# Kernel tuning notes

Hardware: AMD Instinct MI355X
Metric: run time of the kernel (lower is better)

## Reference

```python
import jax, jax.numpy as jnp
import numpy as np

OUT_GRID = (256, 256)  # output_grid_shape


def setup_inputs() -> dict:
    key = jax.random.key(0)
    k1, k2 = jax.random.split(key)
    N, H, W, C = 16, 256, 256, 32
    x = jax.random.normal(k1, (N, H, W, C), dtype=jnp.float32)
    # loc network: global mean pool -> dense(6); small weights + identity-affine bias
    W_loc = jax.random.normal(k2, (C, 6), dtype=jnp.float32) * 0.01
    b_loc = jnp.array([1.0, 0.0, 0.0, 0.0, 1.0, 0.0], dtype=jnp.float32)
    return {"x": x, "W_loc": W_loc, "b_loc": b_loc}


def _spatial_transform(x, W_loc, b_loc):
    N, H, W, C = x.shape
    Ho, Wo = OUT_GRID
    # loc_network: params (N, 6) -> theta (N, 2, 3)
    params = jnp.mean(x, axis=(1, 2)) @ W_loc + b_loc
    theta = params.reshape(N, 2, 3)
    # grid_transform_fn: affine on [-1,1]-normalized output index grid
    gy = jnp.linspace(-1.0, 1.0, Ho, dtype=jnp.float32)
    gx = jnp.linspace(-1.0, 1.0, Wo, dtype=jnp.float32)
    Gy, Gx = jnp.meshgrid(gy, gx, indexing="ij")
    grid = jnp.stack([Gy.ravel(), Gx.ravel(), jnp.ones(Ho * Wo, jnp.float32)], axis=0)  # (3, Ho*Wo)
    coords = jnp.einsum("npq,qm->npm", theta, grid).reshape(N, 2, Ho, Wo)  # in ~[-1,1]
    # interpolate_bilinear with clip (wrap=False)
    maxes = jnp.array([H - 1, W - 1], dtype=jnp.float32)
    up = (coords + 1.0) * maxes[None, :, None, None] * 0.5  # upscale to pixel coords
    f = jnp.floor(up)
    frac = up - f  # (N, 2, Ho, Wo)
    fi = f.astype(jnp.int32)
    batch = jnp.arange(N)[:, None, None]
    out = jnp.zeros((N, Ho, Wo, C), dtype=x.dtype)
    for by in (0, 1):  # 2^dim corner offsets (bitfield)
        for bx in (0, 1):
            cy = jnp.clip(fi[:, 0] + by, 0, H - 1)
            cx = jnp.clip(fi[:, 1] + bx, 0, W - 1)
            wy = frac[:, 0] if by else 1.0 - frac[:, 0]
            wx = frac[:, 1] if bx else 1.0 - frac[:, 1]
            out = out + x[batch, cy, cx] * (wy * wx)[..., None]
    return out


def reference(x, W_loc, b_loc):
    return _spatial_transform(x, W_loc, b_loc)
```

## Files before the change

kernel.cpp:

```cpp
#include <hip/hip_runtime.h>


#define NIMG 16
#define HDIM 256
#define WDIM 256
#define CH   32
#define HW   (HDIM * WDIM)
#define BPI  128

typedef float f32x4 __attribute__((ext_vector_type(4)));

__global__ __launch_bounds__(256) void st_sum_kernel(
    const float* __restrict__ x, float* __restrict__ partials) {
    const int n   = blockIdx.x >> 7;
    const int blk = blockIdx.x & (BPI - 1);
    const int tid = threadIdx.x;
    const int cg  = tid & 7;
    const int sp  = tid >> 3;

    const float4* xp = (const float4*)(x + (size_t)n * HW * CH);
    float4 a0 = make_float4(0.f, 0.f, 0.f, 0.f);
    float4 a1 = make_float4(0.f, 0.f, 0.f, 0.f);
    int s = blk * 32 + sp;
    #pragma unroll
    for (int it = 0; it < 8; ++it) {
        float4 v0 = xp[(size_t)s * 8 + cg];
        float4 v1 = xp[(size_t)(s + BPI * 32) * 8 + cg];
        a0.x += v0.x; a0.y += v0.y; a0.z += v0.z; a0.w += v0.w;
        a1.x += v1.x; a1.y += v1.y; a1.z += v1.z; a1.w += v1.w;
        s += BPI * 64;
    }
    a0.x += a1.x; a0.y += a1.y; a0.z += a1.z; a0.w += a1.w;

    __shared__ float4 red[256];
    red[tid] = a0;
    __syncthreads();
    for (int stride = 16; stride >= 1; stride >>= 1) {
        if (sp < stride) {
            float4 o = red[(sp + stride) * 8 + cg];
            a0.x += o.x; a0.y += o.y; a0.z += o.z; a0.w += o.w;
            red[tid] = a0;
        }
        __syncthreads();
    }
    if (sp == 0) {
        ((float4*)(partials + ((size_t)blk * NIMG + n) * CH))[cg] = a0;
    }
}

__global__ __launch_bounds__(512) void st_theta_kernel(
    const float* __restrict__ partials, const float* __restrict__ W_loc,
    const float* __restrict__ b_loc, float* __restrict__ theta) {
    __shared__ float mean[NIMG * CH];
    const int t = threadIdx.x;
    float s = 0.f;
    for (int b = 0; b < BPI; ++b) s += partials[b * NIMG * CH + t];
    mean[t] = s * (1.0f / (float)HW);
    __syncthreads();
    if (t < NIMG * 6) {
        const int n = t / 6, k = t % 6;
        float acc = b_loc[k];
        for (int c = 0; c < CH; ++c)
            acc = fmaf(mean[n * CH + c], W_loc[c * 6 + k], acc);
        theta[t] = acc;
    }
}

__global__ __launch_bounds__(256) void st_interp_kernel(
    const float* __restrict__ x, const float* __restrict__ theta,
    float* __restrict__ out) {
    const int bid = (int)blockIdx.x;
    const int swz = (bid & 7) * 2048 + (bid >> 3);
    const int n   = swz >> 10;
    const int r   = swz & 1023;
    const int ty  = r >> 4;
    const int tx  = r & 15;
    const int tid = threadIdx.x;
    const int p   = tid >> 3;
    const int cg  = tid & 7;

    const int ho  = ty * 4 + (p >> 3);
    const int wo0 = tx * 16 + (p & 7);
    const int wo1 = wo0 + 8;

    const float* th = theta + n * 6;
    const float t00 = th[0], t01 = th[1], t02 = th[2];
    const float t10 = th[3], t11 = th[4], t12 = th[5];

    const float gy = fmaf((float)ho, 2.0f / 255.0f, -1.0f);
    const float gx0 = fmaf((float)wo0, 2.0f / 255.0f, -1.0f);
    const float gx1 = fmaf((float)wo1, 2.0f / 255.0f, -1.0f);

    const float uyA = (fmaf(t00, gy, fmaf(t01, gx0, t02)) + 1.0f) * 127.5f;
    const float uxA = (fmaf(t10, gy, fmaf(t11, gx0, t12)) + 1.0f) * 127.5f;
    const float uyB = (fmaf(t00, gy, fmaf(t01, gx1, t02)) + 1.0f) * 127.5f;
    const float uxB = (fmaf(t10, gy, fmaf(t11, gx1, t12)) + 1.0f) * 127.5f;

    const float fyA = floorf(uyA), fxA = floorf(uxA);
    const float fyB = floorf(uyB), fxB = floorf(uxB);
    const float ryA = uyA - fyA, rxA = uxA - fxA;
    const float ryB = uyB - fyB, rxB = uxB - fxB;

    const int iyA0 = min(max((int)fyA,     0), HDIM - 1);
    const int iyA1 = min(max((int)fyA + 1, 0), HDIM - 1);
    const int ixA0 = min(max((int)fxA,     0), WDIM - 1);
    const int ixA1 = min(max((int)fxA + 1, 0), WDIM - 1);
    const int iyB0 = min(max((int)fyB,     0), HDIM - 1);
    const int iyB1 = min(max((int)fyB + 1, 0), HDIM - 1);
    const int ixB0 = min(max((int)fxB,     0), WDIM - 1);
    const int ixB1 = min(max((int)fxB + 1, 0), WDIM - 1);

    const float4* xp = (const float4*)(x + (size_t)n * HW * CH);
    float4 a00 = xp[(size_t)(iyA0 * WDIM + ixA0) * 8 + cg];
    float4 a01 = xp[(size_t)(iyA0 * WDIM + ixA1) * 8 + cg];
    float4 a10 = xp[(size_t)(iyA1 * WDIM + ixA0) * 8 + cg];
    float4 a11 = xp[(size_t)(iyA1 * WDIM + ixA1) * 8 + cg];
    float4 b00 = xp[(size_t)(iyB0 * WDIM + ixB0) * 8 + cg];
    float4 b01 = xp[(size_t)(iyB0 * WDIM + ixB1) * 8 + cg];
    float4 b10 = xp[(size_t)(iyB1 * WDIM + ixB0) * 8 + cg];
    float4 b11 = xp[(size_t)(iyB1 * WDIM + ixB1) * 8 + cg];

    const float wA00 = (1.0f - ryA) * (1.0f - rxA);
    const float wA01 = (1.0f - ryA) * rxA;
    const float wA10 = ryA * (1.0f - rxA);
    const float wA11 = ryA * rxA;
    const float wB00 = (1.0f - ryB) * (1.0f - rxB);
    const float wB01 = (1.0f - ryB) * rxB;
    const float wB10 = ryB * (1.0f - rxB);
    const float wB11 = ryB * rxB;

    f32x4 oA, oB;
    oA.x = a00.x * wA00 + a01.x * wA01 + a10.x * wA10 + a11.x * wA11;
    oA.y = a00.y * wA00 + a01.y * wA01 + a10.y * wA10 + a11.y * wA11;
    oA.z = a00.z * wA00 + a01.z * wA01 + a10.z * wA10 + a11.z * wA11;
    oA.w = a00.w * wA00 + a01.w * wA01 + a10.w * wA10 + a11.w * wA11;
    oB.x = b00.x * wB00 + b01.x * wB01 + b10.x * wB10 + b11.x * wB11;
    oB.y = b00.y * wB00 + b01.y * wB01 + b10.y * wB10 + b11.y * wB11;
    oB.z = b00.z * wB00 + b01.z * wB01 + b10.z * wB10 + b11.z * wB11;
    oB.w = b00.w * wB00 + b01.w * wB01 + b10.w * wB10 + b11.w * wB11;

    f32x4* op = (f32x4*)(out + (size_t)n * HW * CH);
    __builtin_nontemporal_store(oA, &op[(size_t)(ho * WDIM + wo0) * 8 + cg]);
    __builtin_nontemporal_store(oB, &op[(size_t)(ho * WDIM + wo1) * 8 + cg]);
}

extern "C" void kernel_launch(void* const* d_in, const int* in_sizes, int n_in,
                              void* d_out, int out_size, void* d_ws, size_t ws_size,
                              hipStream_t stream) {
    const float* x     = (const float*)d_in[0];
    const float* W_loc = (const float*)d_in[1];
    const float* b_loc = (const float*)d_in[2];
    float* out = (float*)d_out;

    float* partials = (float*)d_ws;
    float* theta    = partials + BPI * NIMG * CH;

    st_sum_kernel<<<NIMG * BPI, 256, 0, stream>>>(x, partials);
    st_theta_kernel<<<1, 512, 0, stream>>>(partials, W_loc, b_loc, theta);
    st_interp_kernel<<<NIMG * (HW / 64), 256, 0, stream>>>(x, theta, out);
}
```

Baseline: 68.66 us.

## Fuse theta computation into interpolation kernel and halve sum-kernel block count

Removes the single-block theta kernel launch. Each interpolation block now reduces the per-image partial sums itself and computes its own 6 affine parameters in shared memory. The sum kernel uses 64 blocks per image, each with four independent accumulators, so half as many partials are written. This saves a launch and the serial tail of a one-block kernel, at the cost of redundant partial reads and extra syncs in all 16384 interpolation blocks.

```diff
diff --git a/kernel.cpp b/kernel.cpp
--- a/kernel.cpp
+++ b/kernel.cpp
@@ -6,13 +6,13 @@
 #define WDIM 256
 #define CH   32
 #define HW   (HDIM * WDIM)
-#define BPI  128
+#define BPI  64
 
 typedef float f32x4 __attribute__((ext_vector_type(4)));
 
 __global__ __launch_bounds__(256) void st_sum_kernel(
     const float* __restrict__ x, float* __restrict__ partials) {
-    const int n   = blockIdx.x >> 7;
+    const int n   = blockIdx.x >> 6;
     const int blk = blockIdx.x & (BPI - 1);
     const int tid = threadIdx.x;
     const int cg  = tid & 7;
@@ -21,16 +21,24 @@
     const float4* xp = (const float4*)(x + (size_t)n * HW * CH);
     float4 a0 = make_float4(0.f, 0.f, 0.f, 0.f);
     float4 a1 = make_float4(0.f, 0.f, 0.f, 0.f);
+    float4 a2 = make_float4(0.f, 0.f, 0.f, 0.f);
+    float4 a3 = make_float4(0.f, 0.f, 0.f, 0.f);
     int s = blk * 32 + sp;
     #pragma unroll
     for (int it = 0; it < 8; ++it) {
-        float4 v0 = xp[(size_t)s * 8 + cg];
-        float4 v1 = xp[(size_t)(s + BPI * 32) * 8 + cg];
+        float4 v0 = xp[(size_t)(s       ) * 8 + cg];
+        float4 v1 = xp[(size_t)(s + 2048) * 8 + cg];
+        float4 v2 = xp[(size_t)(s + 4096) * 8 + cg];
+        float4 v3 = xp[(size_t)(s + 6144) * 8 + cg];
         a0.x += v0.x; a0.y += v0.y; a0.z += v0.z; a0.w += v0.w;
         a1.x += v1.x; a1.y += v1.y; a1.z += v1.z; a1.w += v1.w;
-        s += BPI * 64;
+        a2.x += v2.x; a2.y += v2.y; a2.z += v2.z; a2.w += v2.w;
+        a3.x += v3.x; a3.y += v3.y; a3.z += v3.z; a3.w += v3.w;
+        s += 8192;
     }
     a0.x += a1.x; a0.y += a1.y; a0.z += a1.z; a0.w += a1.w;
+    a2.x += a3.x; a2.y += a3.y; a2.z += a3.z; a2.w += a3.w;
+    a0.x += a2.x; a0.y += a2.y; a0.z += a2.z; a0.w += a2.w;
 
     __shared__ float4 red[256];
     red[tid] = a0;
@@ -48,46 +56,54 @@
     }
 }
 
-__global__ __launch_bounds__(512) void st_theta_kernel(
-    const float* __restrict__ partials, const float* __restrict__ W_loc,
-    const float* __restrict__ b_loc, float* __restrict__ theta) {
-    __shared__ float mean[NIMG * CH];
-    const int t = threadIdx.x;
-    float s = 0.f;
-    for (int b = 0; b < BPI; ++b) s += partials[b * NIMG * CH + t];
-    mean[t] = s * (1.0f / (float)HW);
-    __syncthreads();
-    if (t < NIMG * 6) {
-        const int n = t / 6, k = t % 6;
-        float acc = b_loc[k];
-        for (int c = 0; c < CH; ++c)
-            acc = fmaf(mean[n * CH + c], W_loc[c * 6 + k], acc);
-        theta[t] = acc;
-    }
-}
-
 __global__ __launch_bounds__(256) void st_interp_kernel(
-    const float* __restrict__ x, const float* __restrict__ theta,
+    const float* __restrict__ x, const float* __restrict__ partials,
+    const float* __restrict__ W_loc, const float* __restrict__ b_loc,
     float* __restrict__ out) {
     const int bid = (int)blockIdx.x;
     const int swz = (bid & 7) * 2048 + (bid >> 3);
     const int n   = swz >> 10;
     const int r   = swz & 1023;
-    const int ty  = r >> 4;
-    const int tx  = r & 15;
     const int tid = threadIdx.x;
-    const int p   = tid >> 3;
-    const int cg  = tid & 7;
+
+    __shared__ float red2[8][CH];
+    __shared__ float th_s[8];
+    {
+        const int c = tid & 31, g = tid >> 5;
+        float s = 0.f;
+        #pragma unroll
+        for (int j = 0; j < 8; ++j)
+            s += partials[(size_t)((g * 8 + j) * NIMG + n) * CH + c];
+        red2[g][c] = s;
+        __syncthreads();
+        if (g == 0) {
+            float m = 0.f;
+            #pragma unroll
+            for (int j = 0; j < 8; ++j) m += red2[j][c];
+            red2[0][c] = m * (1.0f / (float)HW);
+        }
+        __syncthreads();
+        if (tid < 6) {
+            float acc = b_loc[tid];
+            for (int c2 = 0; c2 < CH; ++c2)
+                acc = fmaf(red2[0][c2], W_loc[c2 * 6 + tid], acc);
+            th_s[tid] = acc;
+        }
+        __syncthreads();
+    }
+    const float t00 = th_s[0], t01 = th_s[1], t02 = th_s[2];
+    const float t10 = th_s[3], t11 = th_s[4], t12 = th_s[5];
+
+    const int ty = r >> 4;
+    const int tx = r & 15;
+    const int p  = tid >> 3;
+    const int cg = tid & 7;
 
     const int ho  = ty * 4 + (p >> 3);
     const int wo0 = tx * 16 + (p & 7);
     const int wo1 = wo0 + 8;
 
-    const float* th = theta + n * 6;
-    const float t00 = th[0], t01 = th[1], t02 = th[2];
-    const float t10 = th[3], t11 = th[4], t12 = th[5];
-
-    const float gy = fmaf((float)ho, 2.0f / 255.0f, -1.0f);
+    const float gy  = fmaf((float)ho,  2.0f / 255.0f, -1.0f);
     const float gx0 = fmaf((float)wo0, 2.0f / 255.0f, -1.0f);
     const float gx1 = fmaf((float)wo1, 2.0f / 255.0f, -1.0f);
 
@@ -153,9 +169,8 @@
     float* out = (float*)d_out;
 
     float* partials = (float*)d_ws;
-    float* theta    = partials + BPI * NIMG * CH;
 
     st_sum_kernel<<<NIMG * BPI, 256, 0, stream>>>(x, partials);
-    st_theta_kernel<<<1, 512, 0, stream>>>(partials, W_loc, b_loc, theta);
-    st_interp_kernel<<<NIMG * (HW / 64), 256, 0, stream>>>(x, theta, out);
+    st_interp_kernel<<<NIMG * (HW / 64), 256, 0, stream>>>(
+        x, partials, W_loc, b_loc, out);
 }
```

Measured after the change: 65.03 us. 1.06x faster.
